# Performance work log

Hardware: AMD Instinct MI355X
Metric: run time of the kernel (lower is better)

## Reference

```python
import jax, jax.numpy as jnp
import numpy as np
from math import sqrt

B, IN_C, OUT_C, H, W, WDIM, K = 16, 512, 512, 64, 64, 512, 3
EPS = 1e-8
LRELU_SLOPE = 0.2


def setup_inputs() -> dict:
    key = jax.random.key(0)
    ks = jax.random.split(key, 5)
    return {
        "x": jax.random.normal(ks[0], (B, IN_C, H, W), dtype=jnp.float32),
        "w": jax.random.normal(ks[1], (B, WDIM), dtype=jnp.float32),
        "noise": jax.random.normal(ks[2], (B, 1, H, W), dtype=jnp.float32),
        "linear_w": jax.random.normal(ks[3], (IN_C, WDIM), dtype=jnp.float32),
        "linear_b": jnp.ones((IN_C,), dtype=jnp.float32),
        "conv_w": jax.random.normal(ks[4], (OUT_C, IN_C, K, K), dtype=jnp.float32),
        "scale_noise": jnp.zeros((OUT_C,), dtype=jnp.float32),
        "bias": jnp.zeros((OUT_C,), dtype=jnp.float32),
    }


def reference(x, w, noise, linear_w, linear_b, conv_w, scale_noise, bias):
    # EqualizerStraights: equalized-lr linear, scale = 1/sqrt(w_dim)
    s = w @ (linear_w * (1.0 / sqrt(WDIM))).T + linear_b  # [b, in_c]
    # Weight_Demod: equalized conv weight, scale = 1/sqrt(in_c*k*k)
    base_w = conv_w * (1.0 / sqrt(IN_C * K * K))  # [out, in, k, k]
    weights = base_w[None] * s[:, None, :, None, None]  # [b, out, in, k, k]
    sigma_inv = jax.lax.rsqrt(
        jnp.sum(weights * weights, axis=(2, 3, 4), keepdims=True) + EPS)
    weights = weights * sigma_inv

    def conv1(xi, wi):  # xi [in,h,w], wi [out,in,k,k]
        return jax.lax.conv_general_dilated(
            xi[None], wi, window_strides=(1, 1), padding="SAME",
            dimension_numbers=("NCHW", "OIHW", "NCHW"))[0]

    y = jax.vmap(conv1)(x, weights)  # [b, out, h, w]
    y = y + scale_noise[None, :, None, None] * noise
    return jax.nn.leaky_relu(y + bias[None, :, None, None], negative_slope=LRELU_SLOPE)
```

## Files before the change

### kernel.cpp

```cpp
#include <hip/hip_runtime.h>
#include <hip/hip_bf16.h>
#include <stdint.h>

typedef __bf16 bf16_t;
typedef __bf16 bf16x8 __attribute__((ext_vector_type(8)));
typedef short short8 __attribute__((ext_vector_type(8)));
typedef float f32x4 __attribute__((ext_vector_type(4)));

#define RS512  0.044194173824159216f
#define RS4608 0.014731391274719739f

__global__ void k_style(const float* __restrict__ w, const float* __restrict__ lw,
                        const float* __restrict__ lb, float* __restrict__ s) {
  int b = blockIdx.y;
  int c = blockIdx.x * 256 + threadIdx.x;
  const float4* wr = (const float4*)(w + b * 512);
  const float4* lr = (const float4*)(lw + (size_t)c * 512);
  float acc = 0.f;
#pragma unroll 4
  for (int d = 0; d < 128; ++d) {
    float4 a = wr[d], q = lr[d];
    acc += a.x * q.x + a.y * q.y + a.z * q.z + a.w * q.w;
  }
  s[b * 512 + c] = acc * RS512 + lb[c];
}

__global__ void k_wprep(const float* __restrict__ cw, float* __restrict__ wsq,
                        bf16_t* __restrict__ bwf, f32x4* __restrict__ zb) {
  if (blockIdx.x == 0) zb[threadIdx.x] = (f32x4)0.f;
  int idx = blockIdx.x * 256 + threadIdx.x;
  int o = idx >> 9, i = idx & 511;
  float v[9];
  float ss = 0.f;
#pragma unroll
  for (int t = 0; t < 9; ++t) {
    float x = cw[(size_t)idx * 9 + t] * RS4608;
    v[t] = x;
    ss += x * x;
  }
  wsq[idx] = ss;
  int lane = (o & 15) | (((i >> 3) & 3) << 4);
  int base_blk = (i >> 5) * 32 + (o >> 4);
#pragma unroll
  for (int t = 0; t < 9; ++t) {
    size_t e = ((size_t)(t * 512 + base_blk) << 9) + lane * 8 + (i & 7);
    bwf[e] = (bf16_t)v[t];
  }
}

__global__ void k_sigma(const float* __restrict__ s, const float* __restrict__ wsq,
                        float* __restrict__ sinv) {
  __shared__ float s2[512];
  int b = blockIdx.y;
  int o = blockIdx.x * 256 + threadIdx.x;
  for (int i = threadIdx.x; i < 512; i += 256) {
    float v = s[b * 512 + i];
    s2[i] = v * v;
  }
  __syncthreads();
  const float4* qr = (const float4*)(wsq + (size_t)o * 512);
  float acc = 0.f;
#pragma unroll 4
  for (int d = 0; d < 128; ++d) {
    float4 q = qr[d];
    acc += q.x * s2[4 * d] + q.y * s2[4 * d + 1] + q.z * s2[4 * d + 2] + q.w * s2[4 * d + 3];
  }
  sinv[b * 512 + o] = rsqrtf(acc + 1e-8f);
}

__global__ void k_xt(const float* __restrict__ x, const float* __restrict__ s,
                     bf16_t* __restrict__ xt) {
  int ic = blockIdx.x, h = blockIdx.y, b = blockIdx.z;
  __shared__ __align__(16) bf16_t tile[8192];
  int t = threadIdx.x;
  int wcol = t & 63;
  int g = t >> 6;
#pragma unroll
  for (int blk = 0; blk < 4; ++blk) {
    int grp = blk * 4 + g;
    bf16x8 vec;
#pragma unroll
    for (int k = 0; k < 8; ++k) {
      int i = ic * 128 + grp * 8 + k;
      float v = x[(((size_t)b * 512 + i) * 64 + h) * 64 + wcol] * s[b * 512 + i];
      vec[k] = (bf16_t)v;
    }
    int chunk = grp ^ (wcol & 15);
    *(bf16x8*)((char*)tile + wcol * 256 + chunk * 16) = vec;
  }
  __syncthreads();
#pragma unroll
  for (int j = 0; j < 4; ++j) {
    int flat = j * 256 + t;
    int wo = flat >> 4, ig8 = flat & 15;
    int chunk = ig8 ^ (wo & 15);
    bf16x8 v = *(bf16x8*)((char*)tile + wo * 256 + chunk * 16);
    int c32 = (ig8 >> 2);
    int slot = (ig8 & 3) ^ ((wo >> 1) & 3);
    *(bf16x8*)(xt + (((size_t)b * 64 + h) * 64 + wo) * 512 + ic * 128 + c32 * 32 + slot * 8) = v;
  }
}

#define AS1 __attribute__((address_space(1)))
#define AS3 __attribute__((address_space(3)))

__device__ __forceinline__ void gl16(const void* g, void* l) {
  __builtin_amdgcn_global_load_lds((const AS1 void*)g, (AS3 void*)l, 16, 0, 0);
}

#define VMCNT(n) asm volatile("s_waitcnt vmcnt(" #n ")" ::: "memory")
#define BAR __builtin_amdgcn_s_barrier()

__global__ __launch_bounds__(256, 2) void k_conv(
    const bf16_t* __restrict__ xt, const bf16_t* __restrict__ bwf,
    const float* __restrict__ sinv, const float* __restrict__ noise,
    const float* __restrict__ snz, const float* __restrict__ bias,
    const char* __restrict__ zb, float* __restrict__ out) {
  __shared__ __align__(16) char lds[81920];

  const int t = threadIdx.x;
  const int rq = blockIdx.x;
  const int OY = blockIdx.y;
  const int b = blockIdx.z;
  const int h0 = rq * 4;
  const int lane = t & 63;
  const int wv = t >> 6;
  const int wm = wv >> 1;
  const int wn = wv & 1;

  const char* xg = (const char*)xt + (size_t)b * 4194304 + (t >> 2) * 1024 + (t & 3) * 16;
  const char* wgp = (const char*)bwf + OY * 8192 + wv * 2048 + lane * 16;
  const char* zgv = zb + t * 16;

  f32x4 acc[4][8] = {};

  const uint32_t woff = (uint32_t)((wm << 12) + (lane << 4));
  uint32_t pX[4][3];
#pragma unroll
  for (int j = 0; j < 4; ++j)
#pragma unroll
    for (int dk = 0; dk < 3; ++dk) {
      int icol = j * 16 + (lane & 15) + dk - 1;
      int ic2 = icol < 0 ? 0 : (icol > 63 ? 63 : icol);
      int slot = (lane >> 4) ^ ((ic2 >> 1) & 3);
      pX[j][dk] = (uint32_t)(32768 + wn * 8192 + ic2 * 64 + slot * 16);
    }
  const bool c0 = (lane & 15) == 0;
  const bool c15 = (lane & 15) == 15;

  auto stW = [&](uint32_t srcoff, uint32_t dst) {
    const char* s0 = wgp + srcoff;
    gl16(s0, lds + dst + (wv << 11));
    gl16(s0 + 1024, lds + dst + (wv << 11) + 1024);
  };
  auto stX = [&](int r, uint32_t cxoff, int xb) {
    int gr = h0 - 1 + r;
    char* d = lds + 32768 + xb * 24576 + r * 4096 + (wv << 10);
    if ((unsigned)gr < 64u) gl16(xg + (size_t)gr * 65536 + cxoff, d);
    else gl16(zgv, d);
  };

  auto CT = [&](int XB, int tap, uint32_t WS) {
    const int ky = tap / 3, kx = tap % 3;
    bf16x8 af[4];
#pragma unroll
    for (int mi = 0; mi < 4; ++mi)
      af[mi] = *(const bf16x8*)(lds + (woff + WS) + (uint32_t)(mi * 1024));
    bf16x8 bfr[8];
#pragma unroll
    for (int ni = 0; ni < 8; ++ni) {
      short8 xv = *(const short8*)(lds + pX[ni & 3][kx] +
                                   (uint32_t)(XB * 24576 + ((ni >> 2) + ky) * 4096));
      if (kx == 0 && (ni & 3) == 0) xv = c0 ? (short8)0 : xv;
      if (kx == 2 && (ni & 3) == 3) xv = c15 ? (short8)0 : xv;
      bfr[ni] = __builtin_bit_cast(bf16x8, xv);
    }
    __builtin_amdgcn_s_setprio(1);
#pragma unroll
    for (int mi = 0; mi < 4; ++mi)
#pragma unroll
      for (int ni = 0; ni < 8; ++ni)
        acc[mi][ni] =
            __builtin_amdgcn_mfma_f32_16x16x32_bf16(af[mi], bfr[ni], acc[mi][ni], 0, 0, 0);
    __builtin_amdgcn_s_setprio(0);
  };

#define UNIT(CWB, CXB, WA, WB, LAST)                                           \
  {                                                                            \
    stW((CWB) + 2u * 524288u, (WB)); stW((CWB) + 3u * 524288u, (WB) + 8192u);  \
    stX(0, (CXB), 1); stX(1, (CXB), 1);                                        \
    CT(0, 0, (WA)); CT(0, 1, (WA) + 8192u);                                    \
    VMCNT(2); BAR;                                                             \
    stW((CWB) + 4u * 524288u, (WA)); stW((CWB) + 5u * 524288u, (WA) + 8192u);  \
    stX(2, (CXB), 1); stX(3, (CXB), 1);                                        \
    CT(0, 2, (WB)); CT(0, 3, (WB) + 8192u);                                    \
    VMCNT(2); BAR;                                                             \
    stW((CWB) + 6u * 524288u, (WB)); stW((CWB) + 7u * 524288u, (WB) + 8192u);  \
    stX(4, (CXB), 1); stX(5, (CXB), 1);                                        \
    CT(0, 4, (WA)); CT(0, 5, (WA) + 8192u);                                    \
    VMCNT(2); BAR;                                                             \
    stW((CWB) + 8u * 524288u, (WA)); stW((CWB) + 32768u, (WA) + 8192u);        \
    CT(0, 6, (WB)); CT(0, 7, (WB) + 8192u);                                    \
    VMCNT(0); BAR;                                                             \
    stW((CWB) + 32768u + 1u * 524288u, (WB));                                  \
    stW((CWB) + 32768u + 2u * 524288u, (WB) + 8192u);                          \
    CT(0, 8, (WA)); CT(1, 0, (WA) + 8192u);                                    \
    VMCNT(0); BAR;                                                             \
    stW((CWB) + 32768u + 3u * 524288u, (WA));                                  \
    stW((CWB) + 32768u + 4u * 524288u, (WA) + 8192u);                          \
    if (!(LAST)) { stX(0, (CXB) + 64u, 0); stX(1, (CXB) + 64u, 0); }           \
    CT(1, 1, (WB)); CT(1, 2, (WB) + 8192u);                                    \
    if (LAST) { VMCNT(0); } else { VMCNT(2); }                                 \
    BAR;                                                                       \
    stW((CWB) + 32768u + 5u * 524288u, (WB));                                  \
    stW((CWB) + 32768u + 6u * 524288u, (WB) + 8192u);                          \
    if (!(LAST)) { stX(2, (CXB) + 64u, 0); stX(3, (CXB) + 64u, 0); }           \
    CT(1, 3, (WA)); CT(1, 4, (WA) + 8192u);                                    \
    if (LAST) { VMCNT(0); } else { VMCNT(2); }                                 \
    BAR;                                                                       \
    stW((CWB) + 32768u + 7u * 524288u, (WA));                                  \
    stW((CWB) + 32768u + 8u * 524288u, (WA) + 8192u);                          \
    if (!(LAST)) { stX(4, (CXB) + 64u, 0); stX(5, (CXB) + 64u, 0); }           \
    CT(1, 5, (WB)); CT(1, 6, (WB) + 8192u);                                    \
    if (LAST) { VMCNT(0); } else { VMCNT(2); }                                 \
    BAR;                                                                       \
    if (!(LAST)) {                                                             \
      stW((CWB) + 65536u, (WB)); stW((CWB) + 65536u + 524288u, (WB) + 8192u);  \
    }                                                                          \
    CT(1, 7, (WA)); CT(1, 8, (WA) + 8192u);                                    \
    if (!(LAST)) { VMCNT(0); BAR; }                                            \
  }

#pragma unroll
  for (int r = 0; r < 6; ++r) stX(r, 0u, 0);
  stW(0u, 0u); stW(524288u, 8192u);
  VMCNT(0); BAR;

  uint32_t cwb = 0, cxb = 64;
#pragma unroll 1
  for (int k = 0; k < 7; ++k) {
    const uint32_t wA = (uint32_t)(k & 1) << 14;
    const uint32_t wB = wA ^ 16384u;
    UNIT(cwb, cxb, wA, wB, 0);
    cwb += 65536u; cxb += 128u;
  }
  UNIT(cwb, cxb, 16384u, 0u, 1);

  const float* sb = sinv + b * 512;
  const int og = OY * 128 + wm * 64 + ((lane >> 4) << 2);
  const int colb = lane & 15;
  float nzv[8];
#pragma unroll
  for (int ni = 0; ni < 8; ++ni) {
    int prow = h0 + wn * 2 + (ni >> 2);
    nzv[ni] = noise[(size_t)b * 4096 + prow * 64 + (ni & 3) * 16 + colb];
  }
#pragma unroll
  for (int mi = 0; mi < 4; ++mi) {
#pragma unroll
    for (int r = 0; r < 4; ++r) {
      int o = og + mi * 16 + r;
      float sv = sb[o];
      float nw = snz[o];
      float bv = bias[o];
      float* obase = out + ((size_t)b * 512 + o) * 4096;
#pragma unroll
      for (int ni = 0; ni < 8; ++ni) {
        int prow = h0 + wn * 2 + (ni >> 2);
        int col = (ni & 3) * 16 + colb;
        float v = acc[mi][ni][r] * sv + nw * nzv[ni] + bv;
        obase[prow * 64 + col] = v > 0.f ? v : 0.2f * v;
      }
    }
  }
}

extern "C" void kernel_launch(void* const* d_in, const int* in_sizes, int n_in,
                              void* d_out, int out_size, void* d_ws, size_t ws_size,
                              hipStream_t stream) {
  const float* x     = (const float*)d_in[0];
  const float* w     = (const float*)d_in[1];
  const float* noise = (const float*)d_in[2];
  const float* lw    = (const float*)d_in[3];
  const float* lb    = (const float*)d_in[4];
  const float* cw    = (const float*)d_in[5];
  const float* snz   = (const float*)d_in[6];
  const float* bias  = (const float*)d_in[7];
  float* out = (float*)d_out;

  char* ws = (char*)d_ws;
  bf16_t* xt   = (bf16_t*)ws;
  bf16_t* bwf  = (bf16_t*)(ws + 67108864);
  float*  s    = (float*)(ws + 71827456);
  float*  sinv = (float*)(ws + 71860224);
  float*  wsq  = (float*)(ws + 71892992);
  char*   zbuf = ws + 72941568;

  k_style<<<dim3(2, 16), 256, 0, stream>>>(w, lw, lb, s);
  k_wprep<<<dim3(1024), 256, 0, stream>>>(cw, wsq, bwf, (f32x4*)zbuf);
  k_sigma<<<dim3(2, 16), 256, 0, stream>>>(s, wsq, sinv);
  k_xt<<<dim3(4, 64, 16), 256, 0, stream>>>(x, s, xt);
  k_conv<<<dim3(16, 4, 16), 256, 0, stream>>>(xt, bwf, sinv, noise, snz, bias, zbuf, out);
}
```

Baseline: 299.7 us.

## Reorder conv taps column-major to reuse X row fragments in registers

Restructures the implicit-GEMM main loop so taps are visited kx-major, letting consecutive ky taps reuse already-loaded X row fragments held in registers (RA/RB rotation), cutting LDS reads of the input tile by about half. The weight staging moves to a three-slot ring with one barrier per tap instead of per two taps, and LDS shrinks from 80KB to 72KB. The trade-off is more barriers and finer-grained vmcnt waits, with a risk of miscounted outstanding loads.

```diff
diff --git a/kernel.cpp b/kernel.cpp
--- a/kernel.cpp
+++ b/kernel.cpp
@@ -111,12 +111,14 @@
 #define VMCNT(n) asm volatile("s_waitcnt vmcnt(" #n ")" ::: "memory")
 #define BAR __builtin_amdgcn_s_barrier()
 
+#define TMAP(jc) ((((jc) % 3) * 3) + ((jc) / 3))
+
 __global__ __launch_bounds__(256, 2) void k_conv(
     const bf16_t* __restrict__ xt, const bf16_t* __restrict__ bwf,
     const float* __restrict__ sinv, const float* __restrict__ noise,
     const float* __restrict__ snz, const float* __restrict__ bias,
     const char* __restrict__ zb, float* __restrict__ out) {
-  __shared__ __align__(16) char lds[81920];
+  __shared__ __align__(16) char lds[73728];
 
   const int t = threadIdx.x;
   const int rq = blockIdx.x;
@@ -133,6 +135,7 @@
   const char* zgv = zb + t * 16;
 
   f32x4 acc[4][8] = {};
+  bf16x8 RA[4], RB[4];
 
   const uint32_t woff = (uint32_t)((wm << 12) + (lane << 4));
   uint32_t pX[4][3];
@@ -143,108 +146,110 @@
       int icol = j * 16 + (lane & 15) + dk - 1;
       int ic2 = icol < 0 ? 0 : (icol > 63 ? 63 : icol);
       int slot = (lane >> 4) ^ ((ic2 >> 1) & 3);
-      pX[j][dk] = (uint32_t)(32768 + wn * 8192 + ic2 * 64 + slot * 16);
+      pX[j][dk] = (uint32_t)(24576 + wn * 8192 + ic2 * 64 + slot * 16);
     }
   const bool c0 = (lane & 15) == 0;
   const bool c15 = (lane & 15) == 15;
 
-  auto stW = [&](uint32_t srcoff, uint32_t dst) {
-    const char* s0 = wgp + srcoff;
-    gl16(s0, lds + dst + (wv << 11));
-    gl16(s0 + 1024, lds + dst + (wv << 11) + 1024);
+  auto stW = [&](uint32_t srcByteOff, int slab) {
+    const char* s0 = wgp + srcByteOff;
+    gl16(s0, lds + slab * 8192 + (wv << 11));
+    gl16(s0 + 1024, lds + slab * 8192 + (wv << 11) + 1024);
   };
   auto stX = [&](int r, uint32_t cxoff, int xb) {
     int gr = h0 - 1 + r;
-    char* d = lds + 32768 + xb * 24576 + r * 4096 + (wv << 10);
+    char* d = lds + 24576 + xb * 24576 + r * 4096 + (wv << 10);
     if ((unsigned)gr < 64u) gl16(xg + (size_t)gr * 65536 + cxoff, d);
     else gl16(zgv, d);
   };
 
-  auto CT = [&](int XB, int tap, uint32_t WS) {
-    const int ky = tap / 3, kx = tap % 3;
-    bf16x8 af[4];
-#pragma unroll
-    for (int mi = 0; mi < 4; ++mi)
-      af[mi] = *(const bf16x8*)(lds + (woff + WS) + (uint32_t)(mi * 1024));
-    bf16x8 bfr[8];
-#pragma unroll
-    for (int ni = 0; ni < 8; ++ni) {
-      short8 xv = *(const short8*)(lds + pX[ni & 3][kx] +
-                                   (uint32_t)(XB * 24576 + ((ni >> 2) + ky) * 4096));
-      if (kx == 0 && (ni & 3) == 0) xv = c0 ? (short8)0 : xv;
-      if (kx == 2 && (ni & 3) == 3) xv = c15 ? (short8)0 : xv;
-      bfr[ni] = __builtin_bit_cast(bf16x8, xv);
-    }
-    __builtin_amdgcn_s_setprio(1);
-#pragma unroll
-    for (int mi = 0; mi < 4; ++mi)
-#pragma unroll
-      for (int ni = 0; ni < 8; ++ni)
-        acc[mi][ni] =
-            __builtin_amdgcn_mfma_f32_16x16x32_bf16(af[mi], bfr[ni], acc[mi][ni], 0, 0, 0);
-    __builtin_amdgcn_s_setprio(0);
-  };
-
-#define UNIT(CWB, CXB, WA, WB, LAST)                                           \
+#define LROW(DST, RREL, KX, XB)                                                \
   {                                                                            \
-    stW((CWB) + 2u * 524288u, (WB)); stW((CWB) + 3u * 524288u, (WB) + 8192u);  \
-    stX(0, (CXB), 1); stX(1, (CXB), 1);                                        \
-    CT(0, 0, (WA)); CT(0, 1, (WA) + 8192u);                                    \
-    VMCNT(2); BAR;                                                             \
-    stW((CWB) + 4u * 524288u, (WA)); stW((CWB) + 5u * 524288u, (WA) + 8192u);  \
-    stX(2, (CXB), 1); stX(3, (CXB), 1);                                        \
-    CT(0, 2, (WB)); CT(0, 3, (WB) + 8192u);                                    \
-    VMCNT(2); BAR;                                                             \
-    stW((CWB) + 6u * 524288u, (WB)); stW((CWB) + 7u * 524288u, (WB) + 8192u);  \
-    stX(4, (CXB), 1); stX(5, (CXB), 1);                                        \
-    CT(0, 4, (WA)); CT(0, 5, (WA) + 8192u);                                    \
-    VMCNT(2); BAR;                                                             \
-    stW((CWB) + 8u * 524288u, (WA)); stW((CWB) + 32768u, (WA) + 8192u);        \
-    CT(0, 6, (WB)); CT(0, 7, (WB) + 8192u);                                    \
-    VMCNT(0); BAR;                                                             \
-    stW((CWB) + 32768u + 1u * 524288u, (WB));                                  \
-    stW((CWB) + 32768u + 2u * 524288u, (WB) + 8192u);                          \
-    CT(0, 8, (WA)); CT(1, 0, (WA) + 8192u);                                    \
-    VMCNT(0); BAR;                                                             \
-    stW((CWB) + 32768u + 3u * 524288u, (WA));                                  \
-    stW((CWB) + 32768u + 4u * 524288u, (WA) + 8192u);                          \
-    if (!(LAST)) { stX(0, (CXB) + 64u, 0); stX(1, (CXB) + 64u, 0); }           \
-    CT(1, 1, (WB)); CT(1, 2, (WB) + 8192u);                                    \
-    if (LAST) { VMCNT(0); } else { VMCNT(2); }                                 \
-    BAR;                                                                       \
-    stW((CWB) + 32768u + 5u * 524288u, (WB));                                  \
-    stW((CWB) + 32768u + 6u * 524288u, (WB) + 8192u);                          \
-    if (!(LAST)) { stX(2, (CXB) + 64u, 0); stX(3, (CXB) + 64u, 0); }           \
-    CT(1, 3, (WA)); CT(1, 4, (WA) + 8192u);                                    \
-    if (LAST) { VMCNT(0); } else { VMCNT(2); }                                 \
-    BAR;                                                                       \
-    stW((CWB) + 32768u + 7u * 524288u, (WA));                                  \
-    stW((CWB) + 32768u + 8u * 524288u, (WA) + 8192u);                          \
-    if (!(LAST)) { stX(4, (CXB) + 64u, 0); stX(5, (CXB) + 64u, 0); }           \
-    CT(1, 5, (WB)); CT(1, 6, (WB) + 8192u);                                    \
-    if (LAST) { VMCNT(0); } else { VMCNT(2); }                                 \
-    BAR;                                                                       \
-    if (!(LAST)) {                                                             \
-      stW((CWB) + 65536u, (WB)); stW((CWB) + 65536u + 524288u, (WB) + 8192u);  \
-    }                                                                          \
-    CT(1, 7, (WA)); CT(1, 8, (WA) + 8192u);                                    \
-    if (!(LAST)) { VMCNT(0); BAR; }                                            \
+    _Pragma("unroll") for (int col = 0; col < 4; ++col) {                      \
+      short8 xv = *(const short8*)(lds + pX[col][(KX)] +                       \
+                                   (uint32_t)((XB) * 24576 + (RREL) * 4096));  \
+      if ((KX) == 0 && col == 0) xv = c0 ? (short8)0 : xv;                     \
+      if ((KX) == 2 && col == 3) xv = c15 ? (short8)0 : xv;                    \
+      DST[col] = __builtin_bit_cast(bf16x8, xv);                               \
+    }                                                                          \
+  }
+
+#define MFMABLK(LO, HI)                                                        \
+  {                                                                            \
+    __builtin_amdgcn_s_setprio(1);                                             \
+    _Pragma("unroll") for (int mi = 0; mi < 4; ++mi) {                         \
+      _Pragma("unroll") for (int col = 0; col < 4; ++col) {                    \
+        acc[mi][col] = __builtin_amdgcn_mfma_f32_16x16x32_bf16(                \
+            af[mi], LO[col], acc[mi][col], 0, 0, 0);                           \
+        acc[mi][col + 4] = __builtin_amdgcn_mfma_f32_16x16x32_bf16(            \
+            af[mi], HI[col], acc[mi][col + 4], 0, 0, 0);                       \
+      }                                                                        \
+    }                                                                          \
+    __builtin_amdgcn_s_setprio(0);                                             \
+  }
+
+#define COMP(JC, XB)                                                           \
+  {                                                                            \
+    bf16x8 af[4];                                                              \
+    _Pragma("unroll") for (int mi = 0; mi < 4; ++mi)                           \
+        af[mi] = *(const bf16x8*)(lds + (uint32_t)(((JC) % 3) * 8192) + woff + \
+                                  (uint32_t)(mi * 1024));                      \
+    if ((JC) % 3 == 0) {                                                       \
+      LROW(RA, 0, (JC) / 3, XB); LROW(RB, 1, (JC) / 3, XB);                    \
+      MFMABLK(RA, RB);                                                         \
+    } else if ((JC) % 3 == 1) {                                                \
+      LROW(RA, 2, (JC) / 3, XB);                                               \
+      MFMABLK(RB, RA);                                                         \
+    } else {                                                                   \
+      LROW(RB, 3, (JC) / 3, XB);                                               \
+      MFMABLK(RA, RB);                                                         \
+    }                                                                          \
+  }
+
+#define PHASE(CWB, CXB, JC, LAST, XB)                                          \
+  {                                                                            \
+    if (!(LAST) && (JC) < 6) stX((JC), (CXB), (XB) ^ 1);                       \
+    if (!(LAST) || (JC) <= 6) {                                                \
+      if ((JC) + 2 <= 8)                                                       \
+        stW((CWB) + (uint32_t)(TMAP((JC) + 2)) * 524288u, ((JC) + 2) % 3);     \
+      else                                                                     \
+        stW((CWB) + 32768u + (uint32_t)(TMAP((JC) - 7)) * 524288u,             \
+            ((JC) + 2) % 3);                                                   \
+    }                                                                          \
+    if (LAST) {                                                                \
+      if ((JC) <= 6) { VMCNT(4); }                                             \
+      else if ((JC) == 7) { VMCNT(2); }                                        \
+      else { VMCNT(0); }                                                       \
+    } else {                                                                   \
+      if ((JC) == 0 || (JC) == 6) { VMCNT(5); }                                \
+      else if ((JC) <= 5) { VMCNT(6); }                                        \
+      else { VMCNT(4); }                                                       \
+    }                                                                          \
+    __builtin_amdgcn_s_barrier();                                              \
+    COMP((JC), (XB));                                                          \
   }
 
 #pragma unroll
   for (int r = 0; r < 6; ++r) stX(r, 0u, 0);
-  stW(0u, 0u); stW(524288u, 8192u);
+  stW(0u * 524288u, 0);
+  stW(3u * 524288u, 1);
   VMCNT(0); BAR;
 
   uint32_t cwb = 0, cxb = 64;
 #pragma unroll 1
-  for (int k = 0; k < 7; ++k) {
-    const uint32_t wA = (uint32_t)(k & 1) << 14;
-    const uint32_t wB = wA ^ 16384u;
-    UNIT(cwb, cxb, wA, wB, 0);
-    cwb += 65536u; cxb += 128u;
-  }
-  UNIT(cwb, cxb, 16384u, 0u, 1);
+  for (int ci = 0; ci < 7; ++ci) {
+#pragma unroll
+    for (int jc = 0; jc < 9; ++jc) PHASE(cwb, cxb, jc, 0, 0);
+    cwb += 32768u; cxb += 64u;
+#pragma unroll
+    for (int jc = 0; jc < 9; ++jc) PHASE(cwb, cxb, jc, 0, 1);
+    cwb += 32768u; cxb += 64u;
+  }
+#pragma unroll
+  for (int jc = 0; jc < 9; ++jc) PHASE(cwb, cxb, jc, 0, 0);
+  cwb += 32768u;
+#pragma unroll
+  for (int jc = 0; jc < 9; ++jc) PHASE(cwb, cxb, jc, 1, 1);
 
   const float* sb = sinv + b * 512;
   const int og = OY * 128 + wm * 64 + ((lane >> 4) << 2);
```

Result: slower. 314.5 us (+4.9%).
